# Performance work log

Measured on AMD Instinct MI355X. Metric: run time of the kernel, lower is better.

Reference implementation:

```python
import jax, jax.numpy as jnp
import numpy as np


def _dwconv3x3(x, w, b):
    # x: [B,C,H,W], w: [C,3,3] depthwise kernel, b: [C]
    out = jax.lax.conv_general_dilated(
        x, w[:, None, :, :], window_strides=(1, 1), padding=((1, 1), (1, 1)),
        dimension_numbers=('NCHW', 'OIHW', 'NCHW'), feature_group_count=x.shape[1])
    return out + b[None, :, None, None]


def setup_inputs() -> dict:
    key = jax.random.key(0)
    B, d_model, H, W = 16, 1024, 64, 64
    L = H * W
    S = 64               # state_dim
    dm2 = d_model // 2
    ks = jax.random.split(key, 6)
    x = jax.random.normal(ks[0], (B, d_model, L), jnp.float32)
    # BCdt_proj: 1x1 conv1d  (d_model//2 -> state_dim)
    w_bcdt = jax.random.normal(ks[1], (S, dm2), jnp.float32) / np.sqrt(dm2).astype(np.float32)
    b_bcdt = jnp.zeros((S,), jnp.float32)
    # dw: depthwise 3x3 conv on state channels
    w_dw = jax.random.normal(ks[2], (S, 3, 3), jnp.float32) * 0.1
    b_dw = jnp.zeros((S,), jnp.float32)
    # A parameter, uniform in [1, 16)
    A = jax.random.uniform(ks[3], (S,), jnp.float32, 1.0, 16.0)
    coeffs = jnp.array([1.0, 0.5, 0.8], jnp.float32)
    # DW: depthwise 3x3 conv on d_model channels
    w_DW = jax.random.normal(ks[4], (d_model, 3, 3), jnp.float32) * 0.1
    b_DW = jnp.zeros((d_model,), jnp.float32)
    return dict(x=x, w_bcdt=w_bcdt, b_bcdt=b_bcdt, w_dw=w_dw, b_dw=b_dw,
                A=A, coeffs=coeffs, w_DW=w_DW, b_DW=b_DW, H=H, W=W)


def reference(x, w_bcdt, b_bcdt, w_dw, b_dw, A, coeffs, w_DW, b_DW, H, W):
    B, d_model, L = x.shape
    dm2 = d_model // 2
    xh, gate = x[:, :dm2, :], x[:, dm2:, :]          # chunk along channels
    # BCdt_proj (1x1 conv1d) then depthwise 3x3 conv over the HxW grid
    BCdt = jnp.einsum('bdl,sd->bsl', xh, w_bcdt) + b_bcdt[None, :, None]
    Sdim = BCdt.shape[1]
    BCdt = _dwconv3x3(BCdt.reshape(B, Sdim, H, W), w_dw, b_dw).reshape(B, Sdim, L)
    # coeff-weighted copies: B_mat, C_mat, dt
    B_mat = coeffs[0] * BCdt
    C_mat = coeffs[1] * BCdt
    dt = coeffs[2] * BCdt
    # softmax over sequence dim L of (dt + A)
    A_soft = jax.nn.softmax(dt + A[None, :, None], axis=-1)
    AB = A_soft * B_mat                               # [B,S,L]
    h = jnp.einsum('bdl,bsl->bds', xh, AB)            # [B,dm2,S]
    y = jnp.einsum('bds,bsl->bdl', h, C_mat)          # [B,dm2,L]
    y = jnp.concatenate([y, gate], axis=1)            # [B,d_model,L]
    y = _dwconv3x3(y.reshape(B, d_model, H, W), w_DW, b_DW)
    return y, h
```

## Files before the change

kernel.cpp:

```cpp
#include <hip/hip_runtime.h>
#include <hip/hip_bf16.h>

typedef __hip_bfloat16 bf16;

#define B_   16
#define DM   1024
#define DM2  512
#define L_   4096
#define S_   64
#define H_   64
#define W_   64

__device__ __forceinline__ float b2f(bf16 v) { return __bfloat162float(v); }

__device__ __forceinline__ float ldv(const void* p, size_t i, bool f32) {
    return f32 ? ((const float*)p)[i] : b2f(((const bf16*)p)[i]);
}
__device__ __forceinline__ void stv(void* p, size_t i, float v, bool f32) {
    if (f32) ((float*)p)[i] = v;
    else     ((bf16*)p)[i] = __float2bfloat16(v);
}

__global__ __launch_bounds__(256) void k_detect(const void* __restrict__ x,
                                                int* __restrict__ flag) {
    const int t = threadIdx.x;
    float v = b2f(((const bf16*)x)[2 * t]);
    bool susp = !(fabsf(v) <= 100.f) || (v != 0.f && fabsf(v) < 1e-20f);
    unsigned long long m = __ballot(susp);
    __shared__ int cnt[4];
    if ((t & 63) == 0) cnt[t >> 6] = __popcll(m);
    __syncthreads();
    if (t == 0) *flag = (cnt[0] + cnt[1] + cnt[2] + cnt[3] > 32) ? 1 : 0;
}

__global__ __launch_bounds__(256, 4) void k_bcdt(const void* __restrict__ x,
                                                 const void* __restrict__ w_bcdt,
                                                 const void* __restrict__ b_bcdt,
                                                 const int* __restrict__ flag,
                                                 float* __restrict__ raw) {
    const bool f32 = (*flag != 0);
    __shared__ alignas(16) float lx[32][68];
    __shared__ alignas(16) float lw[32][68];
    const int tid = threadIdx.x;
    const int l0  = blockIdx.x * 64;
    const int b   = blockIdx.y;
    const int ts  = tid >> 4;
    const int tl  = tid & 15;
    float4 acc[4];
#pragma unroll
    for (int i = 0; i < 4; ++i) acc[i] = make_float4(0.f, 0.f, 0.f, 0.f);
    const size_t xb = (size_t)b * DM * L_;
    for (int dk = 0; dk < DM2; dk += 32) {
#pragma unroll
        for (int k = 0; k < 8; ++k) {
            int i = tid + k * 256;
            int di = i >> 6, li = i & 63;
            lx[di][li] = ldv(x, xb + (size_t)(dk + di) * L_ + l0 + li, f32);
        }
#pragma unroll
        for (int k = 0; k < 8; ++k) {
            int i = tid + k * 256;
            int si = i >> 5, di = i & 31;
            lw[di][si] = ldv(w_bcdt, si * DM2 + dk + di, f32);
        }
        __syncthreads();
#pragma unroll
        for (int d = 0; d < 32; ++d) {
            float4 xv = ((const float4*)lx[d])[tl];
            float4 wv = *(const float4*)&lw[d][ts * 4];
            acc[0].x += wv.x * xv.x; acc[0].y += wv.x * xv.y;
            acc[0].z += wv.x * xv.z; acc[0].w += wv.x * xv.w;
            acc[1].x += wv.y * xv.x; acc[1].y += wv.y * xv.y;
            acc[1].z += wv.y * xv.z; acc[1].w += wv.y * xv.w;
            acc[2].x += wv.z * xv.x; acc[2].y += wv.z * xv.y;
            acc[2].z += wv.z * xv.z; acc[2].w += wv.z * xv.w;
            acc[3].x += wv.w * xv.x; acc[3].y += wv.w * xv.y;
            acc[3].z += wv.w * xv.z; acc[3].w += wv.w * xv.w;
        }
        __syncthreads();
    }
#pragma unroll
    for (int i = 0; i < 4; ++i) {
        int s = ts * 4 + i;
        float bias = ldv(b_bcdt, s, f32);
        acc[i].x += bias; acc[i].y += bias; acc[i].z += bias; acc[i].w += bias;
        ((float4*)(raw + (size_t)(b * S_ + s) * L_ + l0))[tl] = acc[i];
    }
}

__global__ __launch_bounds__(256) void k_dw_s(const float* __restrict__ raw,
                                              const void* __restrict__ w_dw,
                                              const void* __restrict__ b_dw,
                                              const int* __restrict__ flag,
                                              float* __restrict__ conv) {
    const bool f32 = (*flag != 0);
    const int idx = blockIdx.x * 256 + threadIdx.x;
    const int p  = idx & (L_ - 1);
    const int bs = idx >> 12;
    const int s  = bs & (S_ - 1);
    const int i  = p >> 6, j = p & 63;
    const float* src = raw + (size_t)bs * L_;
    float acc = ldv(b_dw, s, f32);
#pragma unroll
    for (int di = 0; di < 3; ++di) {
        int ii = i + di - 1;
        if (ii < 0 || ii >= H_) continue;
#pragma unroll
        for (int dj = 0; dj < 3; ++dj) {
            int jj = j + dj - 1;
            if (jj < 0 || jj >= W_) continue;
            acc += ldv(w_dw, s * 9 + di * 3 + dj, f32) * src[ii * W_ + jj];
        }
    }
    conv[idx] = acc;
}

__global__ __launch_bounds__(256) void k_softmax_ab(const float* __restrict__ conv,
                                                    const void* __restrict__ A,
                                                    const void* __restrict__ coeffs,
                                                    const int* __restrict__ flag,
                                                    float* __restrict__ ab) {
    const bool f32 = (*flag != 0);
    const int row = blockIdx.x;
    const int s   = row & (S_ - 1);
    const int tid = threadIdx.x;
    const float c0 = ldv(coeffs, 0, f32);
    const float c2 = ldv(coeffs, 2, f32);
    const float a  = ldv(A, s, f32);
    const float* src = conv + (size_t)row * L_;
    float v[16];
#pragma unroll
    for (int k = 0; k < 4; ++k) {
        float4 t = ((const float4*)src)[tid * 4 + k];
        v[k * 4 + 0] = t.x; v[k * 4 + 1] = t.y; v[k * 4 + 2] = t.z; v[k * 4 + 3] = t.w;
    }
    float m = -1e30f;
#pragma unroll
    for (int k = 0; k < 16; ++k) m = fmaxf(m, c2 * v[k] + a);
#pragma unroll
    for (int off = 32; off > 0; off >>= 1) m = fmaxf(m, __shfl_down(m, off));
    __shared__ float redm[4], redsum[4];
    const int wv = tid >> 6, lane = tid & 63;
    if (lane == 0) redm[wv] = m;
    __syncthreads();
    m = fmaxf(fmaxf(redm[0], redm[1]), fmaxf(redm[2], redm[3]));
    float e[16];
    float ssum = 0.f;
#pragma unroll
    for (int k = 0; k < 16; ++k) { e[k] = __expf(c2 * v[k] + a - m); ssum += e[k]; }
#pragma unroll
    for (int off = 32; off > 0; off >>= 1) ssum += __shfl_down(ssum, off);
    if (lane == 0) redsum[wv] = ssum;
    __syncthreads();
    ssum = redsum[0] + redsum[1] + redsum[2] + redsum[3];
    const float inv = 1.0f / ssum;
    float* dst = ab + (size_t)row * L_;
#pragma unroll
    for (int k = 0; k < 4; ++k) {
        float4 t;
        t.x = e[k * 4 + 0] * inv * (c0 * v[k * 4 + 0]);
        t.y = e[k * 4 + 1] * inv * (c0 * v[k * 4 + 1]);
        t.z = e[k * 4 + 2] * inv * (c0 * v[k * 4 + 2]);
        t.w = e[k * 4 + 3] * inv * (c0 * v[k * 4 + 3]);
        ((float4*)dst)[tid * 4 + k] = t;
    }
}

__global__ __launch_bounds__(256, 4) void k_hpart(const void* __restrict__ x,
                                                  const float* __restrict__ ab,
                                                  const int* __restrict__ flag,
                                                  float* __restrict__ part) {
    const bool f32 = (*flag != 0);
    __shared__ alignas(16) float xt[32][36];
    __shared__ alignas(16) float at[32][68];
    const int tid = threadIdx.x;
    const int d0  = blockIdx.x * 32;
    const int lc  = blockIdx.y;
    const int b   = blockIdx.z;
    const int tdi = tid >> 4;
    const int tsi = tid & 15;
    float acc[2][4];
#pragma unroll
    for (int i = 0; i < 2; ++i)
#pragma unroll
        for (int j = 0; j < 4; ++j) acc[i][j] = 0.f;
    const size_t xb = (size_t)b * DM * L_ + (size_t)d0 * L_ + lc * 1024;
    const float* abb = ab + (size_t)b * S_ * L_ + lc * 1024;
    for (int l0 = 0; l0 < 1024; l0 += 32) {
#pragma unroll
        for (int k = 0; k < 4; ++k) {
            int i = tid + k * 256;
            int di = i >> 5, li = i & 31;
            xt[li][di] = ldv(x, xb + (size_t)di * L_ + l0 + li, f32);
        }
#pragma unroll
        for (int k = 0; k < 8; ++k) {
            int i = tid + k * 256;
            int si = i >> 5, li = i & 31;
            at[li][si] = abb[(size_t)si * L_ + l0 + li];
        }
        __syncthreads();
#pragma unroll
        for (int l = 0; l < 32; ++l) {
            float2 xv = *(const float2*)&xt[l][tdi * 2];
            float4 av = *(const float4*)&at[l][tsi * 4];
            acc[0][0] += xv.x * av.x; acc[0][1] += xv.x * av.y;
            acc[0][2] += xv.x * av.z; acc[0][3] += xv.x * av.w;
            acc[1][0] += xv.y * av.x; acc[1][1] += xv.y * av.y;
            acc[1][2] += xv.y * av.z; acc[1][3] += xv.y * av.w;
        }
        __syncthreads();
    }
    float* pp = part + ((size_t)lc * B_ + b) * DM2 * S_;
#pragma unroll
    for (int i = 0; i < 2; ++i) {
        int d = d0 + tdi * 2 + i;
        ((float4*)(pp + (size_t)d * S_))[tsi] =
            make_float4(acc[i][0], acc[i][1], acc[i][2], acc[i][3]);
    }
}

__global__ __launch_bounds__(256) void k_hred(const float* __restrict__ part,
                                              const int* __restrict__ flag,
                                              float* __restrict__ hf,
                                              void* __restrict__ out) {
    const bool f32 = (*flag != 0);
    const int idx = blockIdx.x * 256 + threadIdx.x;
    const size_t stride = (size_t)B_ * DM2 * S_;
    float v = part[idx] + part[idx + stride] + part[idx + 2 * stride] + part[idx + 3 * stride];
    hf[idx] = v;
    stv(out, (size_t)B_ * DM * L_ + idx, v, f32);
}

__global__ __launch_bounds__(256) void k_y_ssm(const float* __restrict__ hf,
                                               const float* __restrict__ conv,
                                               const void* __restrict__ coeffs,
                                               const void* __restrict__ wDW,
                                               const void* __restrict__ bDW,
                                               const int* __restrict__ flag,
                                               void* __restrict__ y) {
    const bool f32 = (*flag != 0);
    __shared__ alignas(16) float hsm[16][64];
    __shared__ alignas(16) float convc[8][640];

    const int tid  = threadIdx.x;
    const int lane = tid & 63;
    const int w    = tid >> 6;
    const int c0   = blockIdx.x * 16;
    const int r0   = blockIdx.y * 8;
    const int b    = blockIdx.z;

#pragma unroll
    for (int k = 0; k < 4; ++k) {
        int i = tid + k * 256;
        int c = i >> 6, s = i & 63;
        hsm[c][s] = hf[((size_t)b * DM2 + c0 + c) * S_ + s];
    }

    float acc[4][10];
#pragma unroll
    for (int c = 0; c < 4; ++c)
#pragma unroll
        for (int k = 0; k < 10; ++k) acc[c][k] = 0.f;

    const float* convb = conv + (size_t)b * S_ * L_;
    const int ls  = tid >> 5;
    const int lp  = tid & 31;

    for (int s0 = 0; s0 < S_; s0 += 8) {
        __syncthreads();
#pragma unroll
        for (int k = 0; k < 20; ++k) {
            int p  = lp + 32 * k;
            int gr = r0 - 1 + (p >> 6);
            gr = gr < 0 ? 0 : (gr > 63 ? 63 : gr);
            convc[ls][p] = convb[(size_t)(s0 + ls) * L_ + gr * 64 + (p & 63)];
        }
        __syncthreads();
#pragma unroll
        for (int s = 0; s < 8; ++s) {
            float hv0 = hsm[w * 4 + 0][s0 + s];
            float hv1 = hsm[w * 4 + 1][s0 + s];
            float hv2 = hsm[w * 4 + 2][s0 + s];
            float hv3 = hsm[w * 4 + 3][s0 + s];
#pragma unroll
            for (int k = 0; k < 10; ++k) {
                float cv = convc[s][lane + 64 * k];
                acc[0][k] += hv0 * cv;
                acc[1][k] += hv1 * cv;
                acc[2][k] += hv2 * cv;
                acc[3][k] += hv3 * cv;
            }
        }
    }

    const float c1 = ldv(coeffs, 1, f32);
#pragma unroll
    for (int c4 = 0; c4 < 4; ++c4) {
        const int cl = w * 4 + c4;
        const int c  = c0 + cl;
        float ww[3][3];
#pragma unroll
        for (int di = 0; di < 3; ++di)
#pragma unroll
            for (int dj = 0; dj < 3; ++dj) ww[di][dj] = ldv(wDW, c * 9 + di * 3 + dj, f32);
        const float bias = ldv(bDW, c, f32);

        float vm[10], vl[10], vr[10];
#pragma unroll
        for (int k = 0; k < 10; ++k) {
            int gr = r0 - 1 + k;
            float v = (gr >= 0 && gr < H_) ? acc[c4][k] * c1 : 0.f;
            vm[k] = v;
            float lf = __shfl_up(v, 1);
            float rt = __shfl_down(v, 1);
            vl[k] = (lane > 0)  ? lf : 0.f;
            vr[k] = (lane < 63) ? rt : 0.f;
        }
#pragma unroll
        for (int row = 0; row < 8; ++row) {
            float sum = bias;
#pragma unroll
            for (int di = 0; di < 3; ++di) {
                sum += ww[di][0] * vl[row + di]
                     + ww[di][1] * vm[row + di]
                     + ww[di][2] * vr[row + di];
            }
            stv(y, ((size_t)b * DM + c) * L_ + (r0 + row) * 64 + lane, sum, f32);
        }
    }
}

__global__ __launch_bounds__(256) void k_final_gate(const void* __restrict__ x,
                                                    const void* __restrict__ wDW,
                                                    const void* __restrict__ bDW,
                                                    const int* __restrict__ flag,
                                                    void* __restrict__ y) {
    const bool f32 = (*flag != 0);
    const int lane = threadIdx.x & 63;
    const int w    = threadIdx.x >> 6;
    const int c    = DM2 + blockIdx.x;
    const int b    = blockIdx.y;
    const size_t src = ((size_t)b * DM + c) * L_;

    float ww[3][3];
#pragma unroll
    for (int di = 0; di < 3; ++di)
#pragma unroll
        for (int dj = 0; dj < 3; ++dj) ww[di][dj] = ldv(wDW, c * 9 + di * 3 + dj, f32);
    const float bias = ldv(bDW, c, f32);

    const int r0 = w * 16;
    float vm[18], vl[18], vr[18];
#pragma unroll
    for (int k = 0; k < 18; ++k) {
        int rr = r0 - 1 + k;
        float v = (rr >= 0 && rr < H_) ? ldv(x, src + rr * W_ + lane, f32) : 0.f;
        vm[k] = v;
        float lf = __shfl_up(v, 1);
        float rt = __shfl_down(v, 1);
        vl[k] = (lane > 0)  ? lf : 0.f;
        vr[k] = (lane < 63) ? rt : 0.f;
    }
#pragma unroll
    for (int row = 0; row < 16; ++row) {
        float sum = bias;
#pragma unroll
        for (int di = 0; di < 3; ++di) {
            sum += ww[di][0] * vl[row + di]
                 + ww[di][1] * vm[row + di]
                 + ww[di][2] * vr[row + di];
        }
        stv(y, src + (r0 + row) * W_ + lane, sum, f32);
    }
}

extern "C" void kernel_launch(void* const* d_in, const int* in_sizes, int n_in,
                              void* d_out, int out_size, void* d_ws, size_t ws_size,
                              hipStream_t stream) {
    const void* x      = d_in[0];
    const void* w_bcdt = d_in[1];
    const void* b_bcdt = d_in[2];
    const void* w_dw   = d_in[3];
    const void* b_dw   = d_in[4];
    const void* A      = d_in[5];
    const void* coeffs = d_in[6];
    const void* w_DW   = d_in[7];
    const void* b_DW   = d_in[8];

    char* ws = (char*)d_ws;
    float* f_raw  = (float*)ws;
    float* f_part = (float*)(ws + (size_t)(16 << 20));
    float* f_conv = (float*)(ws + (size_t)(24 << 20));
    float* f_hf   = (float*)(ws + (size_t)(40 << 20));
    int*   flag   = (int*)  (ws + (size_t)(42 << 20));

    k_detect    <<<1,               256, 0, stream>>>(x, flag);
    k_bcdt      <<<dim3(64, 16),    256, 0, stream>>>(x, w_bcdt, b_bcdt, flag, f_raw);
    k_dw_s      <<<16384,           256, 0, stream>>>(f_raw, w_dw, b_dw, flag, f_conv);
    k_softmax_ab<<<1024,            256, 0, stream>>>(f_conv, A, coeffs, flag, f_raw);
    k_hpart     <<<dim3(16, 4, 16), 256, 0, stream>>>(x, f_raw, flag, f_part);
    k_hred      <<<2048,            256, 0, stream>>>(f_part, flag, f_hf, d_out);
    k_y_ssm     <<<dim3(32, 8, 16), 256, 0, stream>>>(f_hf, f_conv, coeffs, w_DW, b_DW, flag, d_out);
    k_final_gate<<<dim3(512, 16),   256, 0, stream>>>(x, w_DW, b_DW, flag, d_out);
}
```

Before: 821.5 us.

## Fuse small depthwise conv with softmax, widen channel tile in y kernel

Merges the state-channel depthwise 3x3 conv and the sequence softmax into one kernel, so each block convolves a whole 64x64 plane in registers using shuffles and then computes the softmax directly. This removes one launch and a full round trip of the conv buffer through global memory. Separately, the y kernel now handles 32 channels per block instead of 16, halving the grid and reusing each staged conv tile across twice as many channels, at the cost of more accumulator registers. The fused kernel reads raw and writes ab into the same buffer, which is safe only because each block reads its plane in full before writing it back.

```diff
diff --git a/kernel.cpp b/kernel.cpp
--- a/kernel.cpp
+++ b/kernel.cpp
@@ -88,81 +88,84 @@
     }
 }
 
-__global__ __launch_bounds__(256) void k_dw_s(const float* __restrict__ raw,
+__global__ __launch_bounds__(256) void k_dwsm(const float* __restrict__ raw,
                                               const void* __restrict__ w_dw,
                                               const void* __restrict__ b_dw,
+                                              const void* __restrict__ A,
+                                              const void* __restrict__ coeffs,
                                               const int* __restrict__ flag,
-                                              float* __restrict__ conv) {
-    const bool f32 = (*flag != 0);
-    const int idx = blockIdx.x * 256 + threadIdx.x;
-    const int p  = idx & (L_ - 1);
-    const int bs = idx >> 12;
-    const int s  = bs & (S_ - 1);
-    const int i  = p >> 6, j = p & 63;
+                                              float* __restrict__ conv,
+                                              float* __restrict__ ab) {
+    const bool f32 = (*flag != 0);
+    const int lane = threadIdx.x & 63;
+    const int w    = threadIdx.x >> 6;
+    const int s    = blockIdx.x;
+    const int b    = blockIdx.y;
+    const int bs   = b * S_ + s;
     const float* src = raw + (size_t)bs * L_;
-    float acc = ldv(b_dw, s, f32);
-#pragma unroll
-    for (int di = 0; di < 3; ++di) {
-        int ii = i + di - 1;
-        if (ii < 0 || ii >= H_) continue;
-#pragma unroll
-        for (int dj = 0; dj < 3; ++dj) {
-            int jj = j + dj - 1;
-            if (jj < 0 || jj >= W_) continue;
-            acc += ldv(w_dw, s * 9 + di * 3 + dj, f32) * src[ii * W_ + jj];
-        }
-    }
-    conv[idx] = acc;
-}
-
-__global__ __launch_bounds__(256) void k_softmax_ab(const float* __restrict__ conv,
-                                                    const void* __restrict__ A,
-                                                    const void* __restrict__ coeffs,
-                                                    const int* __restrict__ flag,
-                                                    float* __restrict__ ab) {
-    const bool f32 = (*flag != 0);
-    const int row = blockIdx.x;
-    const int s   = row & (S_ - 1);
-    const int tid = threadIdx.x;
+
+    float ww[3][3];
+#pragma unroll
+    for (int di = 0; di < 3; ++di)
+#pragma unroll
+        for (int dj = 0; dj < 3; ++dj) ww[di][dj] = ldv(w_dw, s * 9 + di * 3 + dj, f32);
+    const float bias = ldv(b_dw, s, f32);
     const float c0 = ldv(coeffs, 0, f32);
     const float c2 = ldv(coeffs, 2, f32);
     const float a  = ldv(A, s, f32);
-    const float* src = conv + (size_t)row * L_;
-    float v[16];
-#pragma unroll
-    for (int k = 0; k < 4; ++k) {
-        float4 t = ((const float4*)src)[tid * 4 + k];
-        v[k * 4 + 0] = t.x; v[k * 4 + 1] = t.y; v[k * 4 + 2] = t.z; v[k * 4 + 3] = t.w;
-    }
+
+    const int r0 = w * 16;
+    float vm[18], vl[18], vr[18];
+#pragma unroll
+    for (int k = 0; k < 18; ++k) {
+        int rr = r0 - 1 + k;
+        float v = (rr >= 0 && rr < H_) ? src[rr * W_ + lane] : 0.f;
+        vm[k] = v;
+        float lf = __shfl_up(v, 1);
+        float rt = __shfl_down(v, 1);
+        vl[k] = (lane > 0)  ? lf : 0.f;
+        vr[k] = (lane < 63) ? rt : 0.f;
+    }
+    float cv[16];
+#pragma unroll
+    for (int row = 0; row < 16; ++row) {
+        float sum = bias;
+#pragma unroll
+        for (int di = 0; di < 3; ++di) {
+            sum += ww[di][0] * vl[row + di]
+                 + ww[di][1] * vm[row + di]
+                 + ww[di][2] * vr[row + di];
+        }
+        cv[row] = sum;
+    }
+
     float m = -1e30f;
 #pragma unroll
-    for (int k = 0; k < 16; ++k) m = fmaxf(m, c2 * v[k] + a);
+    for (int k = 0; k < 16; ++k) m = fmaxf(m, c2 * cv[k] + a);
 #pragma unroll
     for (int off = 32; off > 0; off >>= 1) m = fmaxf(m, __shfl_down(m, off));
     __shared__ float redm[4], redsum[4];
-    const int wv = tid >> 6, lane = tid & 63;
-    if (lane == 0) redm[wv] = m;
+    if (lane == 0) redm[w] = m;
     __syncthreads();
     m = fmaxf(fmaxf(redm[0], redm[1]), fmaxf(redm[2], redm[3]));
     float e[16];
     float ssum = 0.f;
 #pragma unroll
-    for (int k = 0; k < 16; ++k) { e[k] = __expf(c2 * v[k] + a - m); ssum += e[k]; }
+    for (int k = 0; k < 16; ++k) { e[k] = __expf(c2 * cv[k] + a - m); ssum += e[k]; }
 #pragma unroll
     for (int off = 32; off > 0; off >>= 1) ssum += __shfl_down(ssum, off);
-    if (lane == 0) redsum[wv] = ssum;
+    if (lane == 0) redsum[w] = ssum;
     __syncthreads();
     ssum = redsum[0] + redsum[1] + redsum[2] + redsum[3];
     const float inv = 1.0f / ssum;
-    float* dst = ab + (size_t)row * L_;
-#pragma unroll
-    for (int k = 0; k < 4; ++k) {
-        float4 t;
-        t.x = e[k * 4 + 0] * inv * (c0 * v[k * 4 + 0]);
-        t.y = e[k * 4 + 1] * inv * (c0 * v[k * 4 + 1]);
-        t.z = e[k * 4 + 2] * inv * (c0 * v[k * 4 + 2]);
-        t.w = e[k * 4 + 3] * inv * (c0 * v[k * 4 + 3]);
-        ((float4*)dst)[tid * 4 + k] = t;
+
+    float* cdst = conv + (size_t)bs * L_;
+    float* adst = ab   + (size_t)bs * L_;
+#pragma unroll
+    for (int row = 0; row < 16; ++row) {
+        int p = (r0 + row) * W_ + lane;
+        cdst[p] = cv[row];
+        adst[p] = e[row] * inv * (c0 * cv[row]);
     }
 }
 
@@ -240,26 +243,26 @@
                                                const int* __restrict__ flag,
                                                void* __restrict__ y) {
     const bool f32 = (*flag != 0);
-    __shared__ alignas(16) float hsm[16][64];
+    __shared__ alignas(16) float hsm[32][64];
     __shared__ alignas(16) float convc[8][640];
 
     const int tid  = threadIdx.x;
     const int lane = tid & 63;
     const int w    = tid >> 6;
-    const int c0   = blockIdx.x * 16;
+    const int c0   = blockIdx.x * 32;
     const int r0   = blockIdx.y * 8;
     const int b    = blockIdx.z;
 
 #pragma unroll
-    for (int k = 0; k < 4; ++k) {
+    for (int k = 0; k < 8; ++k) {
         int i = tid + k * 256;
         int c = i >> 6, s = i & 63;
         hsm[c][s] = hf[((size_t)b * DM2 + c0 + c) * S_ + s];
     }
 
-    float acc[4][10];
-#pragma unroll
-    for (int c = 0; c < 4; ++c)
+    float acc[8][10];
+#pragma unroll
+    for (int c = 0; c < 8; ++c)
 #pragma unroll
         for (int k = 0; k < 10; ++k) acc[c][k] = 0.f;
 
@@ -279,25 +282,22 @@
         __syncthreads();
 #pragma unroll
         for (int s = 0; s < 8; ++s) {
-            float hv0 = hsm[w * 4 + 0][s0 + s];
-            float hv1 = hsm[w * 4 + 1][s0 + s];
-            float hv2 = hsm[w * 4 + 2][s0 + s];
-            float hv3 = hsm[w * 4 + 3][s0 + s];
+            float hv[8];
+#pragma unroll
+            for (int c = 0; c < 8; ++c) hv[c] = hsm[w * 8 + c][s0 + s];
 #pragma unroll
             for (int k = 0; k < 10; ++k) {
-                float cv = convc[s][lane + 64 * k];
-                acc[0][k] += hv0 * cv;
-                acc[1][k] += hv1 * cv;
-                acc[2][k] += hv2 * cv;
-                acc[3][k] += hv3 * cv;
+                float cvv = convc[s][lane + 64 * k];
+#pragma unroll
+                for (int c = 0; c < 8; ++c) acc[c][k] += hv[c] * cvv;
             }
         }
     }
 
     const float c1 = ldv(coeffs, 1, f32);
 #pragma unroll
-    for (int c4 = 0; c4 < 4; ++c4) {
-        const int cl = w * 4 + c4;
+    for (int c8 = 0; c8 < 8; ++c8) {
+        const int cl = w * 8 + c8;
         const int c  = c0 + cl;
         float ww[3][3];
 #pragma unroll
@@ -310,7 +310,7 @@
 #pragma unroll
         for (int k = 0; k < 10; ++k) {
             int gr = r0 - 1 + k;
-            float v = (gr >= 0 && gr < H_) ? acc[c4][k] * c1 : 0.f;
+            float v = (gr >= 0 && gr < H_) ? acc[c8][k] * c1 : 0.f;
             vm[k] = v;
             float lf = __shfl_up(v, 1);
             float rt = __shfl_down(v, 1);
@@ -397,10 +397,9 @@
 
     k_detect    <<<1,               256, 0, stream>>>(x, flag);
     k_bcdt      <<<dim3(64, 16),    256, 0, stream>>>(x, w_bcdt, b_bcdt, flag, f_raw);
-    k_dw_s      <<<16384,           256, 0, stream>>>(f_raw, w_dw, b_dw, flag, f_conv);
-    k_softmax_ab<<<1024,            256, 0, stream>>>(f_conv, A, coeffs, flag, f_raw);
+    k_dwsm      <<<dim3(64, 16),    256, 0, stream>>>(f_raw, w_dw, b_dw, A, coeffs, flag, f_conv, f_raw);
     k_hpart     <<<dim3(16, 4, 16), 256, 0, stream>>>(x, f_raw, flag, f_part);
     k_hred      <<<2048,            256, 0, stream>>>(f_part, flag, f_hf, d_out);
-    k_y_ssm     <<<dim3(32, 8, 16), 256, 0, stream>>>(f_hf, f_conv, coeffs, w_DW, b_DW, flag, d_out);
+    k_y_ssm     <<<dim3(16, 8, 16), 256, 0, stream>>>(f_hf, f_conv, coeffs, w_DW, b_DW, flag, d_out);
     k_final_gate<<<dim3(512, 16),   256, 0, stream>>>(x, w_DW, b_DW, flag, d_out);
 }
```

After: 808.0 us. No clear change (-1.6%).
